# Performance work log

Hardware: AMD Instinct MI355X
Metric: run time of the kernel (lower is better)

Reference implementation:

```python
import jax, jax.numpy as jnp
import numpy as np

D_MODEL = 1024
NUM_HEADS = 16
THETA = 10000.0


def setup_inputs() -> dict:
    key = jax.random.key(0)
    ks = jax.random.split(key, 5)
    B, S, D = 4, 2048, D_MODEL
    std = float(np.sqrt(2.0 / (D + D)))
    x = jax.random.normal(ks[0], (B, S, D), dtype=jnp.float32)
    wq = jax.random.normal(ks[1], (D, D), dtype=jnp.float32) * std
    wk = jax.random.normal(ks[2], (D, D), dtype=jnp.float32) * std
    wv = jax.random.normal(ks[3], (D, D), dtype=jnp.float32) * std
    wo = jax.random.normal(ks[4], (D, D), dtype=jnp.float32) * std
    token_positions = jnp.broadcast_to(jnp.arange(S, dtype=jnp.int32), (B, S))
    return {"x": x, "token_positions": token_positions,
            "wq": wq, "wk": wk, "wv": wv, "wo": wo}


def _rope(t, token_positions, d_k):
    # t: [B, H, S, d_k]; token_positions: [B, S]
    freqs = 1.0 / (THETA ** (jnp.arange(0, d_k, 2, dtype=jnp.float32) / d_k))  # [d_k/2]
    angles = token_positions.astype(jnp.float32)[..., None] * freqs            # [B, S, d_k/2]
    angles = jnp.repeat(angles, 2, axis=-1)                                    # [B, S, d_k]
    cos = jnp.cos(angles)[:, None, :, :]  # broadcast over heads
    sin = jnp.sin(angles)[:, None, :, :]
    t1, t2 = t[..., 0::2], t[..., 1::2]
    t_rot = jnp.stack([-t2, t1], axis=-1).reshape(t.shape)  # interleave (-x2, x1)
    return t * cos + t_rot * sin


def reference(x, token_positions, wq, wk, wv, wo):
    B, S, D = x.shape
    H = NUM_HEADS
    d_k = D // H
    def proj(w):
        return (x @ w.T).reshape(B, S, H, d_k).transpose(0, 2, 1, 3)  # [B,H,S,dk]
    q = _rope(proj(wq), token_positions, d_k)
    k = _rope(proj(wk), token_positions, d_k)
    v = proj(wv)
    scale = 1.0 / jnp.sqrt(jnp.float32(d_k))
    scores = jnp.einsum('bhqd,bhkd->bhqk', q, k) * scale  # [B,H,S,S]
    causal = jnp.tril(jnp.ones((S, S), dtype=bool))
    scores = jnp.where(causal, scores, -jnp.inf)
    attn = jax.nn.softmax(scores, axis=-1)
    out = jnp.einsum('bhqk,bhkd->bhqd', attn, v)          # [B,H,S,dk]
    out = out.transpose(0, 2, 1, 3).reshape(B, S, D)
    return out @ wo.T
```

## Files before the change

### kernel.cpp

```cpp
#include <hip/hip_runtime.h>
#include <hip/hip_bf16.h>
#include <cstdint>
#include <cstddef>

#define B_ 4
#define S_ 2048
#define D_ 1024
#define H_ 16
#define DK_ 64
#define NTOK (B_*S_)

typedef __bf16 bf16;
typedef __bf16 bf16x8 __attribute__((ext_vector_type(8)));
typedef short s16x4 __attribute__((ext_vector_type(4)));
typedef float f32x4 __attribute__((ext_vector_type(4)));

#define AS1 __attribute__((address_space(1)))
#define AS3 __attribute__((address_space(3)))

static __device__ __forceinline__ short f2bf_s(float f) {
    return __builtin_bit_cast(short, (__bf16)f);
}

static __device__ __forceinline__ f32x4 mfma16(s16x4 a, s16x4 b, f32x4 c) {
#if __has_builtin(__builtin_amdgcn_mfma_f32_16x16x16bf16_1k)
    return __builtin_amdgcn_mfma_f32_16x16x16bf16_1k(a, b, c, 0, 0, 0);
#else
    asm volatile("v_mfma_f32_16x16x16_bf16 %0, %1, %2, %0\n\ts_nop 7\n\ts_nop 7"
                 : "+v"(c) : "v"(a), "v"(b));
    return c;
#endif
}

__global__ void cvt_all(const float* __restrict__ x, const float* __restrict__ wq,
                        const float* __restrict__ wk, const float* __restrict__ wv,
                        const float* __restrict__ wo, bf16* __restrict__ dst) {
    const int NX8 = NTOK * D_ / 8;
    const int W8 = D_ * D_ / 8;
    int i = blockIdx.x * blockDim.x + threadIdx.x;
    if (i >= NX8 + 4 * W8) return;
    const float* src; int j;
    if (i < NX8) { src = x; j = i; }
    else {
        int k = i - NX8;
        int w = k >> 17;
        j = k & (W8 - 1);
        src = w == 0 ? wq : (w == 1 ? wk : (w == 2 ? wv : wo));
    }
    const float4* s4 = reinterpret_cast<const float4*>(src) + (size_t)j * 2;
    float4 a = s4[0], b = s4[1];
    bf16x8 o;
    o[0] = (bf16)a.x; o[1] = (bf16)a.y; o[2] = (bf16)a.z; o[3] = (bf16)a.w;
    o[4] = (bf16)b.x; o[5] = (bf16)b.y; o[6] = (bf16)b.z; o[7] = (bf16)b.w;
    reinterpret_cast<bf16x8*>(dst)[i] = o;
}

__global__ void rope_table(const int* __restrict__ pos, float2* __restrict__ tab) {
    int i = blockIdx.x * blockDim.x + threadIdx.x;
    if (i >= NTOK * 32) return;
    int n = i >> 5, p = i & 31;
    float pf = (float)pos[n];
    float freq = powf(10000.0f, -(float)p * (1.0f / 32.0f));
    float ang = pf * freq;
    float s, c;
    sincosf(ang, &s, &c);
    tab[i] = make_float2(c, s);
}

__global__ __launch_bounds__(256, 2)
void gemm_qkv(const bf16* __restrict__ A, const bf16* __restrict__ Bw,
              bf16* __restrict__ Qr, bf16* __restrict__ Kz, bf16* __restrict__ VT,
              const float2* __restrict__ tab) {
    const float SCL2E = 0.125f * 1.44269504088896340736f;
    constexpr int NKT = 16;
    __shared__ alignas(16) bf16 lds[2][(128 + 128) * 64];
    const int tid = threadIdx.x;
    const int lane = tid & 63;
    const int wid = tid >> 6;
    const int wm = wid >> 1, wn = wid & 1;
    const int lr = lane & 15, lg = lane >> 4;
    const int m0 = blockIdx.x * 128;
    const int n0g = blockIdx.y * 128;

    f32x4 acc[4][4] = {};

    auto stageA = [&](int kt, int bufi) {
        bf16* dst = &lds[bufi][0];
#pragma unroll
        for (int j = 0; j < 4; ++j) {
            int flat = j * 256 + tid;
            int r = flat >> 3, c = flat & 7;
            const bf16* src = A + (size_t)(m0 + r) * 1024 + kt * 64 + ((c ^ (r & 7)) << 3);
            __builtin_amdgcn_global_load_lds((const AS1 uint32_t*)src,
                                             (AS3 uint32_t*)(dst + (size_t)flat * 8), 16, 0, 0);
        }
    };
    auto stageB = [&](int kt, int bufi) {
        bf16* dst = &lds[bufi][0] + 128 * 64;
#pragma unroll
        for (int j = 0; j < 4; ++j) {
            int flat = j * 256 + tid;
            int r = flat >> 3, c = flat & 7;
            const bf16* src = Bw + (size_t)(n0g + r) * 1024 + kt * 64 + ((c ^ (r & 7)) << 3);
            __builtin_amdgcn_global_load_lds((const AS1 uint32_t*)src,
                                             (AS3 uint32_t*)(dst + (size_t)flat * 8), 16, 0, 0);
        }
    };

    stageA(0, 0);
    stageB(0, 0);

    for (int kt = 0; kt < NKT; ++kt) {
        const bf16* bufA = &lds[kt & 1][0];
        const bf16* bufB = bufA + 128 * 64;

        asm volatile("" ::: "memory");
        __builtin_amdgcn_s_barrier();
        asm volatile("" ::: "memory");
        if (kt + 1 < NKT) {
            stageA(kt + 1, (kt + 1) & 1);
            asm volatile("s_waitcnt vmcnt(4)" ::: "memory");
        } else {
            asm volatile("s_waitcnt vmcnt(0)" ::: "memory");
        }
        __builtin_amdgcn_s_barrier();
        asm volatile("" ::: "memory");

        const int sx = lr & 7;
        bf16x8 af[4][2], bfr[4][2];
#pragma unroll
        for (int mf = 0; mf < 4; ++mf)
#pragma unroll
            for (int kh = 0; kh < 2; ++kh)
                af[mf][kh] = *reinterpret_cast<const bf16x8*>(
                    &bufA[(wm * 64 + mf * 16 + lr) * 64 + (((kh * 4 + lg) ^ sx) << 3)]);
#pragma unroll
        for (int nf = 0; nf < 2; ++nf)
#pragma unroll
            for (int kh = 0; kh < 2; ++kh)
                bfr[nf][kh] = *reinterpret_cast<const bf16x8*>(
                    &bufB[(wn * 64 + nf * 16 + lr) * 64 + (((kh * 4 + lg) ^ sx) << 3)]);
        __builtin_amdgcn_s_setprio(1);
#pragma unroll
        for (int mf = 0; mf < 4; ++mf)
#pragma unroll
            for (int nf = 0; nf < 2; ++nf)
#pragma unroll
                for (int kh = 0; kh < 2; ++kh)
                    acc[mf][nf] = __builtin_amdgcn_mfma_f32_16x16x32_bf16(af[mf][kh], bfr[nf][kh], acc[mf][nf], 0, 0, 0);
        __builtin_amdgcn_s_setprio(0);
        if (kt + 1 < NKT) stageB(kt + 1, (kt + 1) & 1);
        asm volatile("" ::: "memory");
        __builtin_amdgcn_s_barrier();
        asm volatile("" ::: "memory");
#pragma unroll
        for (int nf = 2; nf < 4; ++nf)
#pragma unroll
            for (int kh = 0; kh < 2; ++kh)
                bfr[nf][kh] = *reinterpret_cast<const bf16x8*>(
                    &bufB[(wn * 64 + nf * 16 + lr) * 64 + (((kh * 4 + lg) ^ sx) << 3)]);
        __builtin_amdgcn_s_setprio(1);
#pragma unroll
        for (int mf = 0; mf < 4; ++mf)
#pragma unroll
            for (int nf = 2; nf < 4; ++nf)
#pragma unroll
                for (int kh = 0; kh < 2; ++kh)
                    acc[mf][nf] = __builtin_amdgcn_mfma_f32_16x16x32_bf16(af[mf][kh], bfr[nf][kh], acc[mf][nf], 0, 0, 0);
        __builtin_amdgcn_s_setprio(0);
    }

#pragma unroll
    for (int mf = 0; mf < 4; ++mf) {
#pragma unroll
        for (int nf = 0; nf < 4; ++nf) {
            int row0 = m0 + wm * 64 + mf * 16 + lg * 4;
            int colg = n0g + wn * 64 + nf * 16 + lr;
            int which = colg >> 10;
            int col = colg & 1023;
            if (which < 2) {
#pragma unroll
                for (int r = 0; r < 4; ++r) {
                    int row = row0 + r;
                    float v = acc[mf][nf][r];
                    float partner = __shfl_xor(v, 1, 64);
                    float2 cs = tab[(size_t)row * 32 + ((col >> 1) & 31)];
                    float o = (col & 1) ? fmaf(v, cs.x, partner * cs.y)
                                        : fmaf(v, cs.x, -partner * cs.y);
                    if (which == 0) {
                        Qr[(size_t)row * 1024 + col] = (bf16)(o * SCL2E);
                    } else {
                        int h = col >> 6, e = col & 63;
                        int e2 = e ^ ((row & 7) << 3);
                        Kz[(size_t)row * 1024 + h * 64 + e2] = (bf16)o;
                    }
                }
            } else {
                int h = col >> 6, dd = col & 63;
                int kvb = row0 & 63;
                int sw = (((dd & 7) ^ ((dd >> 3) & 7)) & 7) << 3;
                s16x4 pk;
#pragma unroll
                for (int r = 0; r < 4; ++r) pk[r] = f2bf_s(acc[mf][nf][r]);
                size_t addr = ((((size_t)((row0 >> 11) * 16 + h)) * 32 + ((row0 >> 6) & 31)) * 64 + dd) * 64
                              + (size_t)(kvb ^ sw);
                *reinterpret_cast<s16x4*>(&VT[addr]) = pk;
            }
        }
    }
}

__global__ __launch_bounds__(256, 2)
void gemm_out(const bf16* __restrict__ A, const bf16* __restrict__ Bw,
              float* __restrict__ Cp) {
    constexpr int NKT = 16;
    __shared__ alignas(16) bf16 lds[2][(128 + 128) * 64];
    const int tid = threadIdx.x;
    const int lane = tid & 63;
    const int wid = tid >> 6;
    const int wm = wid >> 1, wn = wid & 1;
    const int lr = lane & 15, lg = lane >> 4;
    const int m0 = blockIdx.x * 128;
    const int n0g = blockIdx.y * 128;

    f32x4 acc[4][4] = {};

    auto stageA = [&](int kt, int bufi) {
        bf16* dst = &lds[bufi][0];
#pragma unroll
        for (int j = 0; j < 4; ++j) {
            int flat = j * 256 + tid;
            int r = flat >> 3, c = flat & 7;
            const bf16* src = A + (size_t)(m0 + r) * 1024 + kt * 64 + ((c ^ (r & 7)) << 3);
            __builtin_amdgcn_global_load_lds((const AS1 uint32_t*)src,
                                             (AS3 uint32_t*)(dst + (size_t)flat * 8), 16, 0, 0);
        }
    };
    auto stageB = [&](int kt, int bufi) {
        bf16* dst = &lds[bufi][0] + 128 * 64;
#pragma unroll
        for (int j = 0; j < 4; ++j) {
            int flat = j * 256 + tid;
            int r = flat >> 3, c = flat & 7;
            const bf16* src = Bw + (size_t)(n0g + r) * 1024 + kt * 64 + ((c ^ (r & 7)) << 3);
            __builtin_amdgcn_global_load_lds((const AS1 uint32_t*)src,
                                             (AS3 uint32_t*)(dst + (size_t)flat * 8), 16, 0, 0);
        }
    };

    stageA(0, 0);
    stageB(0, 0);

    for (int kt = 0; kt < NKT; ++kt) {
        const bf16* bufA = &lds[kt & 1][0];
        const bf16* bufB = bufA + 128 * 64;

        asm volatile("" ::: "memory");
        __builtin_amdgcn_s_barrier();
        asm volatile("" ::: "memory");
        if (kt + 1 < NKT) {
            stageA(kt + 1, (kt + 1) & 1);
            asm volatile("s_waitcnt vmcnt(4)" ::: "memory");
        } else {
            asm volatile("s_waitcnt vmcnt(0)" ::: "memory");
        }
        __builtin_amdgcn_s_barrier();
        asm volatile("" ::: "memory");

        const int sx = lr & 7;
        bf16x8 af[4][2], bfr[4][2];
#pragma unroll
        for (int mf = 0; mf < 4; ++mf)
#pragma unroll
            for (int kh = 0; kh < 2; ++kh)
                af[mf][kh] = *reinterpret_cast<const bf16x8*>(
                    &bufA[(wm * 64 + mf * 16 + lr) * 64 + (((kh * 4 + lg) ^ sx) << 3)]);
#pragma unroll
        for (int nf = 0; nf < 2; ++nf)
#pragma unroll
            for (int kh = 0; kh < 2; ++kh)
                bfr[nf][kh] = *reinterpret_cast<const bf16x8*>(
                    &bufB[(wn * 64 + nf * 16 + lr) * 64 + (((kh * 4 + lg) ^ sx) << 3)]);
        __builtin_amdgcn_s_setprio(1);
#pragma unroll
        for (int mf = 0; mf < 4; ++mf)
#pragma unroll
            for (int nf = 0; nf < 2; ++nf)
#pragma unroll
                for (int kh = 0; kh < 2; ++kh)
                    acc[mf][nf] = __builtin_amdgcn_mfma_f32_16x16x32_bf16(af[mf][kh], bfr[nf][kh], acc[mf][nf], 0, 0, 0);
        __builtin_amdgcn_s_setprio(0);
        if (kt + 1 < NKT) stageB(kt + 1, (kt + 1) & 1);
        asm volatile("" ::: "memory");
        __builtin_amdgcn_s_barrier();
        asm volatile("" ::: "memory");
#pragma unroll
        for (int nf = 2; nf < 4; ++nf)
#pragma unroll
            for (int kh = 0; kh < 2; ++kh)
                bfr[nf][kh] = *reinterpret_cast<const bf16x8*>(
                    &bufB[(wn * 64 + nf * 16 + lr) * 64 + (((kh * 4 + lg) ^ sx) << 3)]);
        __builtin_amdgcn_s_setprio(1);
#pragma unroll
        for (int mf = 0; mf < 4; ++mf)
#pragma unroll
            for (int nf = 2; nf < 4; ++nf)
#pragma unroll
                for (int kh = 0; kh < 2; ++kh)
                    acc[mf][nf] = __builtin_amdgcn_mfma_f32_16x16x32_bf16(af[mf][kh], bfr[nf][kh], acc[mf][nf], 0, 0, 0);
        __builtin_amdgcn_s_setprio(0);
    }

#pragma unroll
    for (int mf = 0; mf < 4; ++mf)
#pragma unroll
        for (int nf = 0; nf < 4; ++nf)
#pragma unroll
            for (int r = 0; r < 4; ++r) {
                int row = m0 + wm * 64 + mf * 16 + lg * 4 + r;
                int colg = n0g + wn * 64 + nf * 16 + lr;
                Cp[(size_t)row * 1024 + colg] = acc[mf][nf][r];
            }
}

__global__ __launch_bounds__(256, 2)
void flash_attn11(const bf16* __restrict__ Q, const bf16* __restrict__ Kz,
                  const bf16* __restrict__ VT, bf16* __restrict__ O) {
    __shared__ bf16 Ks[2][64 * 64];
    __shared__ bf16 Vt[2][64 * 64];
    const int tid = threadIdx.x, lane = tid & 63, w = tid >> 6;
    const int lr = lane & 15, lg = lane >> 4;
    const int qtA = blockIdx.x;
    const int qtB = 15 - qtA;
    const int q0[2] = { qtA * 128, qtB * 128 };
    const int ntS[2] = { 2 * qtA + 2, 2 * qtB + 2 };
    const int NT = ntS[1];
    const int bh = blockIdx.y;
    const int b = bh >> 4, h = bh & 15;
    const size_t base = ((size_t)b * S_) * D_ + (size_t)h * DK_;
    const size_t vtbase = (size_t)bh * 32 * 4096;

    bf16x8 aq[2][2][2];
#pragma unroll
    for (int si = 0; si < 2; ++si)
#pragma unroll
        for (int qs = 0; qs < 2; ++qs) {
            int qrow = q0[si] + w * 32 + qs * 16 + lr;
            const bf16* qp = Q + base + (size_t)qrow * D_ + lg * 8;
            aq[si][qs][0] = *reinterpret_cast<const bf16x8*>(qp);
            aq[si][qs][1] = *reinterpret_cast<const bf16x8*>(qp + 32);
        }

    f32x4 acc[2][2][4] = {};
    f32x4 l_acc[2][2] = {};
    float m_run[2][2] = {{-1e30f, -1e30f}, {-1e30f, -1e30f}};

    const short ONEB = (short)0x3F80;
    const s16x4 ones = { ONEB, ONEB, ONEB, ONEB };

    const int sjj = tid >> 3;
    const int se0 = (tid & 7) * 8;

    auto stage = [&](int t, int bufi) {
        bf16* kd = Ks[bufi];
        bf16* vd = Vt[bufi];
#pragma unroll
        for (int i = 0; i < 2; ++i) {
            int jj = sjj + i * 32;
            const bf16* ksrc = Kz + base + (size_t)(t * 64 + jj) * 1024 + se0;
            __builtin_amdgcn_global_load_lds((const AS1 uint32_t*)ksrc,
                                             (AS3 uint32_t*)(kd + jj * 64 + se0), 16, 0, 0);
            const bf16* vsrc = VT + vtbase + (size_t)t * 4096 + jj * 64 + se0;
            __builtin_amdgcn_global_load_lds((const AS1 uint32_t*)vsrc,
                                             (AS3 uint32_t*)(vd + jj * 64 + se0), 16, 0, 0);
        }
    };

    stage(0, 0);

    for (int t = 0; t < NT; ++t) {
        const int j0 = t * 64;
        const bf16* KsB = Ks[t & 1];
        const bf16* VtB = Vt[t & 1];

        asm volatile("" ::: "memory");
        __builtin_amdgcn_s_barrier();
        asm volatile("" ::: "memory");
        if (t + 1 < NT) {
            stage(t + 1, (t + 1) & 1);
            asm volatile("s_waitcnt vmcnt(4)" ::: "memory");
        } else {
            asm volatile("s_waitcnt vmcnt(0)" ::: "memory");
        }
        __builtin_amdgcn_s_barrier();
        asm volatile("" ::: "memory");

        const bool act[2] = { t < ntS[0] && j0 <= q0[0] + w * 32 + 31,
                              j0 <= q0[1] + w * 32 + 31 };
        f32x4 sc[2][2][4];

        __builtin_amdgcn_s_setprio(1);
#pragma unroll
        for (int si = 0; si < 2; ++si) {
            if (!act[si]) continue;
#pragma unroll
            for (int nt = 0; nt < 4; ++nt) {
                int krow = nt * 16 + lr;
                int swz = (krow & 7) << 3;
                bf16x8 a0 = *reinterpret_cast<const bf16x8*>(&KsB[krow * 64 + ((lg * 8) ^ swz)]);
                bf16x8 a1 = *reinterpret_cast<const bf16x8*>(&KsB[krow * 64 + ((32 + lg * 8) ^ swz)]);
#pragma unroll
                for (int qs = 0; qs < 2; ++qs) {
                    f32x4 tv = {};
                    tv = __builtin_amdgcn_mfma_f32_16x16x32_bf16(a0, aq[si][qs][0], tv, 0, 0, 0);
                    tv = __builtin_amdgcn_mfma_f32_16x16x32_bf16(a1, aq[si][qs][1], tv, 0, 0, 0);
                    sc[si][qs][nt] = tv;
                }
            }
        }
        __builtin_amdgcn_s_setprio(0);

#pragma unroll
        for (int si = 0; si < 2; ++si) {
            if (!act[si]) continue;

            s16x4 ap[2][4];
#pragma unroll
            for (int qs = 0; qs < 2; ++qs) {
                const int qrow = q0[si] + w * 32 + qs * 16 + lr;
                if (j0 + 63 > q0[si] + w * 32 + qs * 16) {
#pragma unroll
                    for (int nt = 0; nt < 4; ++nt)
#pragma unroll
                        for (int r = 0; r < 4; ++r) {
                            int kv = j0 + nt * 16 + lg * 4 + r;
                            if (kv > qrow) sc[si][qs][nt][r] = -1e30f;
                        }
                }
                float tmax = sc[si][qs][0][0];
#pragma unroll
                for (int nt = 0; nt < 4; ++nt)
#pragma unroll
                    for (int r = 0; r < 4; ++r) tmax = fmaxf(tmax, sc[si][qs][nt][r]);
                tmax = fmaxf(tmax, __shfl_xor(tmax, 16, 64));
                tmax = fmaxf(tmax, __shfl_xor(tmax, 32, 64));
                float mold = m_run[si][qs];
                if (!__all(tmax - mold <= 8.0f)) {
                    float mnew = fmaxf(mold, tmax);
                    float corr = exp2f(mold - mnew);
                    m_run[si][qs] = mnew;
#pragma unroll
                    for (int r = 0; r < 4; ++r) {
                        float cr = __shfl(corr, (lane & 48) | (lg * 4 + r), 64);
                        l_acc[si][qs][r] *= cr;
#pragma unroll
                        for (int dt = 0; dt < 4; ++dt) acc[si][qs][dt][r] *= cr;
                    }
                }
                float mnow = m_run[si][qs];
#pragma unroll
                for (int nt = 0; nt < 4; ++nt) {
                    float p0 = exp2f(sc[si][qs][nt][0] - mnow);
                    float p1 = exp2f(sc[si][qs][nt][1] - mnow);
                    float p2 = exp2f(sc[si][qs][nt][2] - mnow);
                    float p3 = exp2f(sc[si][qs][nt][3] - mnow);
                    int ulo, uhi;
                    asm("v_cvt_pk_bf16_f32 %0, %1, %2" : "=v"(ulo) : "v"(p0), "v"(p1));
                    asm("v_cvt_pk_bf16_f32 %0, %1, %2" : "=v"(uhi) : "v"(p2), "v"(p3));
                    int2 pr; pr.x = ulo; pr.y = uhi;
                    ap[qs][nt] = __builtin_bit_cast(s16x4, pr);
                }
            }

            __builtin_amdgcn_s_setprio(1);
#pragma unroll
            for (int qs = 0; qs < 2; ++qs)
#pragma unroll
                for (int nt = 0; nt < 4; ++nt)
                    l_acc[si][qs] = mfma16(ap[qs][nt], ones, l_acc[si][qs]);
#pragma unroll
            for (int dt = 0; dt < 4; ++dt) {
                int vrow = dt * 16 + lr;
                int vswz = (((vrow & 7) ^ (vrow >> 3)) & 7) << 3;
                s16x4 bv[4];
#pragma unroll
                for (int nt = 0; nt < 4; ++nt)
                    bv[nt] = *reinterpret_cast<const s16x4*>(&VtB[vrow * 64 + ((nt * 16 + lg * 4) ^ vswz)]);
#pragma unroll
                for (int qs = 0; qs < 2; ++qs)
#pragma unroll
                    for (int nt = 0; nt < 4; ++nt)
                        acc[si][qs][dt] = mfma16(ap[qs][nt], bv[nt], acc[si][qs][dt]);
            }
            __builtin_amdgcn_s_setprio(0);
        }
    }

#pragma unroll
    for (int si = 0; si < 2; ++si)
#pragma unroll
        for (int qs = 0; qs < 2; ++qs)
#pragma unroll
            for (int r = 0; r < 4; ++r) {
                float invr = __builtin_amdgcn_rcpf(l_acc[si][qs][r]);
                int row = q0[si] + w * 32 + qs * 16 + lg * 4 + r;
#pragma unroll
                for (int dt = 0; dt < 4; ++dt)
                    O[base + (size_t)row * D_ + dt * 16 + lr] = (bf16)(acc[si][qs][dt][r] * invr);
            }
}

extern "C" void kernel_launch(void* const* d_in, const int* in_sizes, int n_in,
                              void* d_out, int out_size, void* d_ws, size_t ws_size,
                              hipStream_t stream) {
    const float* x  = (const float*)d_in[0];
    const int*   tp = (const int*)d_in[1];
    const float* wq = (const float*)d_in[2];
    const float* wk = (const float*)d_in[3];
    const float* wv = (const float*)d_in[4];
    const float* wo = (const float*)d_in[5];

    bf16* ws = (bf16*)d_ws;
    bf16* Xbf = ws;
    bf16* Wqb = Xbf + (size_t)NTOK * D_;
    bf16* Wkb = Wqb + (size_t)D_ * D_;
    bf16* Wvb = Wkb + (size_t)D_ * D_;
    bf16* Wob = Wvb + (size_t)D_ * D_;
    bf16* Qr  = Wob + (size_t)D_ * D_;
    bf16* Kz  = Qr + (size_t)NTOK * D_;
    bf16* VT  = Kz + (size_t)NTOK * D_;
    bf16* AO  = VT + (size_t)NTOK * D_;
    float2* tab = (float2*)(AO + (size_t)NTOK * D_);
    (void)ws_size; (void)in_sizes; (void)n_in; (void)out_size;
    (void)Wkb; (void)Wvb;

    {
        int ntot8 = (NTOK * D_ + 4 * D_ * D_) / 8;
        cvt_all<<<(ntot8 + 255) / 256, 256, 0, stream>>>(x, wq, wk, wv, wo, Xbf);
    }
    rope_table<<<(NTOK * 32 + 255) / 256, 256, 0, stream>>>(tp, tab);

    gemm_qkv<<<dim3(NTOK / 128, 24), 256, 0, stream>>>(Xbf, Wqb, Qr, Kz, VT, tab);

    flash_attn11<<<dim3(8, B_ * H_), 256, 0, stream>>>(Qr, Kz, VT, AO);

    gemm_out<<<dim3(NTOK / 128, D_ / 128), 256, 0, stream>>>(AO, Wob, (float*)d_out);
}
```

Baseline: 206.9 us.

## Split attention work over 8 waves per block and merge cvt with rope table

The flash attention kernel now launches 512 threads per block, so each wave handles 16 query rows per tile instead of 32. This halves per-thread register state and raises the number of waves available to hide latency. Only the first 256 threads issue the K/V LDS staging loads. Separately, the bf16 conversion and RoPE table kernels are merged into one launch to save a kernel launch. The risks are lower MFMA reuse of each K/V fragment per wave and heavier barrier synchronisation across 8 waves.

```diff
diff --git a/kernel.cpp b/kernel.cpp
--- a/kernel.cpp
+++ b/kernel.cpp
@@ -32,39 +32,40 @@
 #endif
 }
 
-__global__ void cvt_all(const float* __restrict__ x, const float* __restrict__ wq,
-                        const float* __restrict__ wk, const float* __restrict__ wv,
-                        const float* __restrict__ wo, bf16* __restrict__ dst) {
+__global__ void cvt_rope(const float* __restrict__ x, const float* __restrict__ wq,
+                         const float* __restrict__ wk, const float* __restrict__ wv,
+                         const float* __restrict__ wo, const int* __restrict__ pos,
+                         bf16* __restrict__ dst, float2* __restrict__ tab) {
     const int NX8 = NTOK * D_ / 8;
     const int W8 = D_ * D_ / 8;
+    const int NCVT = NX8 + 4 * W8;
     int i = blockIdx.x * blockDim.x + threadIdx.x;
-    if (i >= NX8 + 4 * W8) return;
-    const float* src; int j;
-    if (i < NX8) { src = x; j = i; }
-    else {
-        int k = i - NX8;
-        int w = k >> 17;
-        j = k & (W8 - 1);
-        src = w == 0 ? wq : (w == 1 ? wk : (w == 2 ? wv : wo));
-    }
-    const float4* s4 = reinterpret_cast<const float4*>(src) + (size_t)j * 2;
-    float4 a = s4[0], b = s4[1];
-    bf16x8 o;
-    o[0] = (bf16)a.x; o[1] = (bf16)a.y; o[2] = (bf16)a.z; o[3] = (bf16)a.w;
-    o[4] = (bf16)b.x; o[5] = (bf16)b.y; o[6] = (bf16)b.z; o[7] = (bf16)b.w;
-    reinterpret_cast<bf16x8*>(dst)[i] = o;
-}
-
-__global__ void rope_table(const int* __restrict__ pos, float2* __restrict__ tab) {
-    int i = blockIdx.x * blockDim.x + threadIdx.x;
-    if (i >= NTOK * 32) return;
-    int n = i >> 5, p = i & 31;
-    float pf = (float)pos[n];
-    float freq = powf(10000.0f, -(float)p * (1.0f / 32.0f));
-    float ang = pf * freq;
-    float s, c;
-    sincosf(ang, &s, &c);
-    tab[i] = make_float2(c, s);
+    if (i < NCVT) {
+        const float* src; int j;
+        if (i < NX8) { src = x; j = i; }
+        else {
+            int k = i - NX8;
+            int w = k >> 17;
+            j = k & (W8 - 1);
+            src = w == 0 ? wq : (w == 1 ? wk : (w == 2 ? wv : wo));
+        }
+        const float4* s4 = reinterpret_cast<const float4*>(src) + (size_t)j * 2;
+        float4 a = s4[0], b = s4[1];
+        bf16x8 o;
+        o[0] = (bf16)a.x; o[1] = (bf16)a.y; o[2] = (bf16)a.z; o[3] = (bf16)a.w;
+        o[4] = (bf16)b.x; o[5] = (bf16)b.y; o[6] = (bf16)b.z; o[7] = (bf16)b.w;
+        reinterpret_cast<bf16x8*>(dst)[i] = o;
+    } else {
+        int k = i - NCVT;
+        if (k >= NTOK * 32) return;
+        int n = k >> 5, p = k & 31;
+        float pf = (float)pos[n];
+        float freq = powf(10000.0f, -(float)p * (1.0f / 32.0f));
+        float ang = pf * freq;
+        float s, c;
+        sincosf(ang, &s, &c);
+        tab[k] = make_float2(c, s);
+    }
 }
 
 __global__ __launch_bounds__(256, 2)
@@ -323,8 +324,8 @@
             }
 }
 
-__global__ __launch_bounds__(256, 2)
-void flash_attn11(const bf16* __restrict__ Q, const bf16* __restrict__ Kz,
+__global__ __launch_bounds__(512)
+void flash_attn13(const bf16* __restrict__ Q, const bf16* __restrict__ Kz,
                   const bf16* __restrict__ VT, bf16* __restrict__ O) {
     __shared__ bf16 Ks[2][64 * 64];
     __shared__ bf16 Vt[2][64 * 64];
@@ -340,28 +341,28 @@
     const size_t base = ((size_t)b * S_) * D_ + (size_t)h * DK_;
     const size_t vtbase = (size_t)bh * 32 * 4096;
 
-    bf16x8 aq[2][2][2];
-#pragma unroll
-    for (int si = 0; si < 2; ++si)
-#pragma unroll
-        for (int qs = 0; qs < 2; ++qs) {
-            int qrow = q0[si] + w * 32 + qs * 16 + lr;
-            const bf16* qp = Q + base + (size_t)qrow * D_ + lg * 8;
-            aq[si][qs][0] = *reinterpret_cast<const bf16x8*>(qp);
-            aq[si][qs][1] = *reinterpret_cast<const bf16x8*>(qp + 32);
-        }
-
-    f32x4 acc[2][2][4] = {};
-    f32x4 l_acc[2][2] = {};
-    float m_run[2][2] = {{-1e30f, -1e30f}, {-1e30f, -1e30f}};
+    bf16x8 aq[2][2];
+#pragma unroll
+    for (int si = 0; si < 2; ++si) {
+        int qrow = q0[si] + w * 16 + lr;
+        const bf16* qp = Q + base + (size_t)qrow * D_ + lg * 8;
+        aq[si][0] = *reinterpret_cast<const bf16x8*>(qp);
+        aq[si][1] = *reinterpret_cast<const bf16x8*>(qp + 32);
+    }
+
+    f32x4 acc[2][4] = {};
+    f32x4 l_acc[2] = {};
+    float m_run[2] = {-1e30f, -1e30f};
 
     const short ONEB = (short)0x3F80;
     const s16x4 ones = { ONEB, ONEB, ONEB, ONEB };
 
     const int sjj = tid >> 3;
     const int se0 = (tid & 7) * 8;
+    const bool stager = tid < 256;
 
     auto stage = [&](int t, int bufi) {
+        if (!stager) return;
         bf16* kd = Ks[bufi];
         bf16* vd = Vt[bufi];
 #pragma unroll
@@ -395,89 +396,76 @@
         __builtin_amdgcn_s_barrier();
         asm volatile("" ::: "memory");
 
-        const bool act[2] = { t < ntS[0] && j0 <= q0[0] + w * 32 + 31,
-                              j0 <= q0[1] + w * 32 + 31 };
-        f32x4 sc[2][2][4];
-
-        __builtin_amdgcn_s_setprio(1);
 #pragma unroll
         for (int si = 0; si < 2; ++si) {
-            if (!act[si]) continue;
+            if (t >= ntS[si]) continue;
+            const int qw0 = q0[si] + w * 16;
+            if (j0 > qw0 + 15) continue;
+
+            f32x4 sc[4];
+            __builtin_amdgcn_s_setprio(1);
 #pragma unroll
             for (int nt = 0; nt < 4; ++nt) {
                 int krow = nt * 16 + lr;
                 int swz = (krow & 7) << 3;
                 bf16x8 a0 = *reinterpret_cast<const bf16x8*>(&KsB[krow * 64 + ((lg * 8) ^ swz)]);
                 bf16x8 a1 = *reinterpret_cast<const bf16x8*>(&KsB[krow * 64 + ((32 + lg * 8) ^ swz)]);
-#pragma unroll
-                for (int qs = 0; qs < 2; ++qs) {
-                    f32x4 tv = {};
-                    tv = __builtin_amdgcn_mfma_f32_16x16x32_bf16(a0, aq[si][qs][0], tv, 0, 0, 0);
-                    tv = __builtin_amdgcn_mfma_f32_16x16x32_bf16(a1, aq[si][qs][1], tv, 0, 0, 0);
-                    sc[si][qs][nt] = tv;
+                f32x4 tv = {};
+                tv = __builtin_amdgcn_mfma_f32_16x16x32_bf16(a0, aq[si][0], tv, 0, 0, 0);
+                tv = __builtin_amdgcn_mfma_f32_16x16x32_bf16(a1, aq[si][1], tv, 0, 0, 0);
+                sc[nt] = tv;
+            }
+            __builtin_amdgcn_s_setprio(0);
+
+            const int qrow = qw0 + lr;
+            if (j0 + 63 > qw0) {
+#pragma unroll
+                for (int nt = 0; nt < 4; ++nt)
+#pragma unroll
+                    for (int r = 0; r < 4; ++r) {
+                        int kv = j0 + nt * 16 + lg * 4 + r;
+                        if (kv > qrow) sc[nt][r] = -1e30f;
+                    }
+            }
+            float tmax = sc[0][0];
+#pragma unroll
+            for (int nt = 0; nt < 4; ++nt)
+#pragma unroll
+                for (int r = 0; r < 4; ++r) tmax = fmaxf(tmax, sc[nt][r]);
+            tmax = fmaxf(tmax, __shfl_xor(tmax, 16, 64));
+            tmax = fmaxf(tmax, __shfl_xor(tmax, 32, 64));
+            float mold = m_run[si];
+            if (!__all(tmax - mold <= 8.0f)) {
+                float mnew = fmaxf(mold, tmax);
+                float corr = exp2f(mold - mnew);
+                m_run[si] = mnew;
+#pragma unroll
+                for (int r = 0; r < 4; ++r) {
+                    float cr = __shfl(corr, (lane & 48) | (lg * 4 + r), 64);
+                    l_acc[si][r] *= cr;
+#pragma unroll
+                    for (int dt = 0; dt < 4; ++dt) acc[si][dt][r] *= cr;
                 }
             }
-        }
-        __builtin_amdgcn_s_setprio(0);
-
-#pragma unroll
-        for (int si = 0; si < 2; ++si) {
-            if (!act[si]) continue;
-
-            s16x4 ap[2][4];
-#pragma unroll
-            for (int qs = 0; qs < 2; ++qs) {
-                const int qrow = q0[si] + w * 32 + qs * 16 + lr;
-                if (j0 + 63 > q0[si] + w * 32 + qs * 16) {
-#pragma unroll
-                    for (int nt = 0; nt < 4; ++nt)
-#pragma unroll
-                        for (int r = 0; r < 4; ++r) {
-                            int kv = j0 + nt * 16 + lg * 4 + r;
-                            if (kv > qrow) sc[si][qs][nt][r] = -1e30f;
-                        }
-                }
-                float tmax = sc[si][qs][0][0];
-#pragma unroll
-                for (int nt = 0; nt < 4; ++nt)
-#pragma unroll
-                    for (int r = 0; r < 4; ++r) tmax = fmaxf(tmax, sc[si][qs][nt][r]);
-                tmax = fmaxf(tmax, __shfl_xor(tmax, 16, 64));
-                tmax = fmaxf(tmax, __shfl_xor(tmax, 32, 64));
-                float mold = m_run[si][qs];
-                if (!__all(tmax - mold <= 8.0f)) {
-                    float mnew = fmaxf(mold, tmax);
-                    float corr = exp2f(mold - mnew);
-                    m_run[si][qs] = mnew;
-#pragma unroll
-                    for (int r = 0; r < 4; ++r) {
-                        float cr = __shfl(corr, (lane & 48) | (lg * 4 + r), 64);
-                        l_acc[si][qs][r] *= cr;
-#pragma unroll
-                        for (int dt = 0; dt < 4; ++dt) acc[si][qs][dt][r] *= cr;
-                    }
-                }
-                float mnow = m_run[si][qs];
-#pragma unroll
-                for (int nt = 0; nt < 4; ++nt) {
-                    float p0 = exp2f(sc[si][qs][nt][0] - mnow);
-                    float p1 = exp2f(sc[si][qs][nt][1] - mnow);
-                    float p2 = exp2f(sc[si][qs][nt][2] - mnow);
-                    float p3 = exp2f(sc[si][qs][nt][3] - mnow);
-                    int ulo, uhi;
-                    asm("v_cvt_pk_bf16_f32 %0, %1, %2" : "=v"(ulo) : "v"(p0), "v"(p1));
-                    asm("v_cvt_pk_bf16_f32 %0, %1, %2" : "=v"(uhi) : "v"(p2), "v"(p3));
-                    int2 pr; pr.x = ulo; pr.y = uhi;
-                    ap[qs][nt] = __builtin_bit_cast(s16x4, pr);
-                }
+            float mnow = m_run[si];
+            s16x4 ap[4];
+#pragma unroll
+            for (int nt = 0; nt < 4; ++nt) {
+                float p0 = exp2f(sc[nt][0] - mnow);
+                float p1 = exp2f(sc[nt][1] - mnow);
+                float p2 = exp2f(sc[nt][2] - mnow);
+                float p3 = exp2f(sc[nt][3] - mnow);
+                int ulo, uhi;
+                asm("v_cvt_pk_bf16_f32 %0, %1, %2" : "=v"(ulo) : "v"(p0), "v"(p1));
+                asm("v_cvt_pk_bf16_f32 %0, %1, %2" : "=v"(uhi) : "v"(p2), "v"(p3));
+                int2 pr; pr.x = ulo; pr.y = uhi;
+                ap[nt] = __builtin_bit_cast(s16x4, pr);
             }
 
             __builtin_amdgcn_s_setprio(1);
 #pragma unroll
-            for (int qs = 0; qs < 2; ++qs)
-#pragma unroll
-                for (int nt = 0; nt < 4; ++nt)
-                    l_acc[si][qs] = mfma16(ap[qs][nt], ones, l_acc[si][qs]);
+            for (int nt = 0; nt < 4; ++nt)
+                l_acc[si] = mfma16(ap[nt], ones, l_acc[si]);
 #pragma unroll
             for (int dt = 0; dt < 4; ++dt) {
                 int vrow = dt * 16 + lr;
@@ -487,10 +475,8 @@
                 for (int nt = 0; nt < 4; ++nt)
                     bv[nt] = *reinterpret_cast<const s16x4*>(&VtB[vrow * 64 + ((nt * 16 + lg * 4) ^ vswz)]);
 #pragma unroll
-                for (int qs = 0; qs < 2; ++qs)
-#pragma unroll
-                    for (int nt = 0; nt < 4; ++nt)
-                        acc[si][qs][dt] = mfma16(ap[qs][nt], bv[nt], acc[si][qs][dt]);
+                for (int nt = 0; nt < 4; ++nt)
+                    acc[si][dt] = mfma16(ap[nt], bv[nt], acc[si][dt]);
             }
             __builtin_amdgcn_s_setprio(0);
         }
@@ -499,15 +485,13 @@
 #pragma unroll
     for (int si = 0; si < 2; ++si)
 #pragma unroll
-        for (int qs = 0; qs < 2; ++qs)
-#pragma unroll
-            for (int r = 0; r < 4; ++r) {
-                float invr = __builtin_amdgcn_rcpf(l_acc[si][qs][r]);
-                int row = q0[si] + w * 32 + qs * 16 + lg * 4 + r;
-#pragma unroll
-                for (int dt = 0; dt < 4; ++dt)
-                    O[base + (size_t)row * D_ + dt * 16 + lr] = (bf16)(acc[si][qs][dt][r] * invr);
-            }
+        for (int r = 0; r < 4; ++r) {
+            float invr = __builtin_amdgcn_rcpf(l_acc[si][r]);
+            int row = q0[si] + w * 16 + lg * 4 + r;
+#pragma unroll
+            for (int dt = 0; dt < 4; ++dt)
+                O[base + (size_t)row * D_ + dt * 16 + lr] = (bf16)(acc[si][dt][r] * invr);
+        }
 }
 
 extern "C" void kernel_launch(void* const* d_in, const int* in_sizes, int n_in,
@@ -535,14 +519,13 @@
     (void)Wkb; (void)Wvb;
 
     {
-        int ntot8 = (NTOK * D_ + 4 * D_ * D_) / 8;
-        cvt_all<<<(ntot8 + 255) / 256, 256, 0, stream>>>(x, wq, wk, wv, wo, Xbf);
-    }
-    rope_table<<<(NTOK * 32 + 255) / 256, 256, 0, stream>>>(tp, tab);
+        int ntot = (NTOK * D_ + 4 * D_ * D_) / 8 + NTOK * 32;
+        cvt_rope<<<(ntot + 255) / 256, 256, 0, stream>>>(x, wq, wk, wv, wo, tp, Xbf, tab);
+    }
 
     gemm_qkv<<<dim3(NTOK / 128, 24), 256, 0, stream>>>(Xbf, Wqb, Qr, Kz, VT, tab);
 
-    flash_attn11<<<dim3(8, B_ * H_), 256, 0, stream>>>(Qr, Kz, VT, AO);
+    flash_attn13<<<dim3(8, B_ * H_), 512, 0, stream>>>(Qr, Kz, VT, AO);
 
     gemm_out<<<dim3(NTOK / 128, D_ / 128), 256, 0, stream>>>(AO, Wob, (float*)d_out);
 }
```

New measurement: 219.6 us. 6.2% more time.

## Stage 128-key KV tiles per barrier in attention and fuse rope table into convert

Applied to the files above, without the earlier changes.

The flash attention kernel now stages two 64-key K/V tiles (128 keys) into LDS per double-buffer step. This halves the number of barrier/wait rounds and issues larger load batches, at the cost of doubling LDS use to 64KB per block, which may limit occupancy. Separately, the rope sin/cos table computation is merged into the bf16 conversion kernel to drop one launch.

```diff
diff --git a/kernel.cpp b/kernel.cpp
--- a/kernel.cpp
+++ b/kernel.cpp
@@ -32,39 +32,40 @@
 #endif
 }
 
-__global__ void cvt_all(const float* __restrict__ x, const float* __restrict__ wq,
-                        const float* __restrict__ wk, const float* __restrict__ wv,
-                        const float* __restrict__ wo, bf16* __restrict__ dst) {
+__global__ void cvt_rope(const float* __restrict__ x, const float* __restrict__ wq,
+                         const float* __restrict__ wk, const float* __restrict__ wv,
+                         const float* __restrict__ wo, const int* __restrict__ pos,
+                         bf16* __restrict__ dst, float2* __restrict__ tab) {
     const int NX8 = NTOK * D_ / 8;
     const int W8 = D_ * D_ / 8;
+    const int NCVT = NX8 + 4 * W8;
     int i = blockIdx.x * blockDim.x + threadIdx.x;
-    if (i >= NX8 + 4 * W8) return;
-    const float* src; int j;
-    if (i < NX8) { src = x; j = i; }
-    else {
-        int k = i - NX8;
-        int w = k >> 17;
-        j = k & (W8 - 1);
-        src = w == 0 ? wq : (w == 1 ? wk : (w == 2 ? wv : wo));
+    if (i < NCVT) {
+        const float* src; int j;
+        if (i < NX8) { src = x; j = i; }
+        else {
+            int k = i - NX8;
+            int w = k >> 17;
+            j = k & (W8 - 1);
+            src = w == 0 ? wq : (w == 1 ? wk : (w == 2 ? wv : wo));
+        }
+        const float4* s4 = reinterpret_cast<const float4*>(src) + (size_t)j * 2;
+        float4 a = s4[0], b = s4[1];
+        bf16x8 o;
+        o[0] = (bf16)a.x; o[1] = (bf16)a.y; o[2] = (bf16)a.z; o[3] = (bf16)a.w;
+        o[4] = (bf16)b.x; o[5] = (bf16)b.y; o[6] = (bf16)b.z; o[7] = (bf16)b.w;
+        reinterpret_cast<bf16x8*>(dst)[i] = o;
+    } else {
+        int k = i - NCVT;
+        if (k >= NTOK * 32) return;
+        int n = k >> 5, p = k & 31;
+        float pf = (float)pos[n];
+        float freq = powf(10000.0f, -(float)p * (1.0f / 32.0f));
+        float ang = pf * freq;
+        float s, c;
+        sincosf(ang, &s, &c);
+        tab[k] = make_float2(c, s);
     }
-    const float4* s4 = reinterpret_cast<const float4*>(src) + (size_t)j * 2;
-    float4 a = s4[0], b = s4[1];
-    bf16x8 o;
-    o[0] = (bf16)a.x; o[1] = (bf16)a.y; o[2] = (bf16)a.z; o[3] = (bf16)a.w;
-    o[4] = (bf16)b.x; o[5] = (bf16)b.y; o[6] = (bf16)b.z; o[7] = (bf16)b.w;
-    reinterpret_cast<bf16x8*>(dst)[i] = o;
-}
-
-__global__ void rope_table(const int* __restrict__ pos, float2* __restrict__ tab) {
-    int i = blockIdx.x * blockDim.x + threadIdx.x;
-    if (i >= NTOK * 32) return;
-    int n = i >> 5, p = i & 31;
-    float pf = (float)pos[n];
-    float freq = powf(10000.0f, -(float)p * (1.0f / 32.0f));
-    float ang = pf * freq;
-    float s, c;
-    sincosf(ang, &s, &c);
-    tab[i] = make_float2(c, s);
 }
 
 __global__ __launch_bounds__(256, 2)
@@ -324,10 +325,10 @@
 }
 
 __global__ __launch_bounds__(256, 2)
-void flash_attn11(const bf16* __restrict__ Q, const bf16* __restrict__ Kz,
+void flash_attn15(const bf16* __restrict__ Q, const bf16* __restrict__ Kz,
                   const bf16* __restrict__ VT, bf16* __restrict__ O) {
-    __shared__ bf16 Ks[2][64 * 64];
-    __shared__ bf16 Vt[2][64 * 64];
+    __shared__ bf16 Ks[2][128 * 64];
+    __shared__ bf16 Vt[2][2 * 4096];
     const int tid = threadIdx.x, lane = tid & 63, w = tid >> 6;
     const int lr = lane & 15, lg = lane >> 4;
     const int qtA = blockIdx.x;
@@ -335,6 +336,7 @@
     const int q0[2] = { qtA * 128, qtB * 128 };
     const int ntS[2] = { 2 * qtA + 2, 2 * qtB + 2 };
     const int NT = ntS[1];
+    const int NT2 = NT >> 1;
     const int bh = blockIdx.y;
     const int b = bh >> 4, h = bh & 15;
     const size_t base = ((size_t)b * S_) * D_ + (size_t)h * DK_;
@@ -361,138 +363,143 @@
     const int sjj = tid >> 3;
     const int se0 = (tid & 7) * 8;
 
-    auto stage = [&](int t, int bufi) {
+    auto stage = [&](int t2, int bufi) {
         bf16* kd = Ks[bufi];
         bf16* vd = Vt[bufi];
 #pragma unroll
-        for (int i = 0; i < 2; ++i) {
+        for (int i = 0; i < 4; ++i) {
             int jj = sjj + i * 32;
-            const bf16* ksrc = Kz + base + (size_t)(t * 64 + jj) * 1024 + se0;
+            const bf16* ksrc = Kz + base + (size_t)(t2 * 128 + jj) * 1024 + se0;
             __builtin_amdgcn_global_load_lds((const AS1 uint32_t*)ksrc,
                                              (AS3 uint32_t*)(kd + jj * 64 + se0), 16, 0, 0);
-            const bf16* vsrc = VT + vtbase + (size_t)t * 4096 + jj * 64 + se0;
-            __builtin_amdgcn_global_load_lds((const AS1 uint32_t*)vsrc,
-                                             (AS3 uint32_t*)(vd + jj * 64 + se0), 16, 0, 0);
-        }
+        }
+#pragma unroll
+        for (int s2 = 0; s2 < 2; ++s2)
+#pragma unroll
+            for (int i = 0; i < 2; ++i) {
+                int jj = sjj + i * 32;
+                const bf16* vsrc = VT + vtbase + (size_t)(t2 * 2 + s2) * 4096 + jj * 64 + se0;
+                __builtin_amdgcn_global_load_lds((const AS1 uint32_t*)vsrc,
+                                                 (AS3 uint32_t*)(vd + s2 * 4096 + jj * 64 + se0), 16, 0, 0);
+            }
     };
 
     stage(0, 0);
 
-    for (int t = 0; t < NT; ++t) {
-        const int j0 = t * 64;
-        const bf16* KsB = Ks[t & 1];
-        const bf16* VtB = Vt[t & 1];
-
-        asm volatile("" ::: "memory");
-        __builtin_amdgcn_s_barrier();
-        asm volatile("" ::: "memory");
-        if (t + 1 < NT) {
-            stage(t + 1, (t + 1) & 1);
-            asm volatile("s_waitcnt vmcnt(4)" ::: "memory");
+    for (int t2 = 0; t2 < NT2; ++t2) {
+        asm volatile("" ::: "memory");
+        __builtin_amdgcn_s_barrier();
+        asm volatile("" ::: "memory");
+        if (t2 + 1 < NT2) {
+            stage(t2 + 1, (t2 + 1) & 1);
+            asm volatile("s_waitcnt vmcnt(8)" ::: "memory");
         } else {
             asm volatile("s_waitcnt vmcnt(0)" ::: "memory");
         }
         __builtin_amdgcn_s_barrier();
         asm volatile("" ::: "memory");
 
-        const bool act[2] = { t < ntS[0] && j0 <= q0[0] + w * 32 + 31,
-                              j0 <= q0[1] + w * 32 + 31 };
-        f32x4 sc[2][2][4];
-
-        __builtin_amdgcn_s_setprio(1);
-#pragma unroll
-        for (int si = 0; si < 2; ++si) {
-            if (!act[si]) continue;
-#pragma unroll
-            for (int nt = 0; nt < 4; ++nt) {
-                int krow = nt * 16 + lr;
-                int swz = (krow & 7) << 3;
-                bf16x8 a0 = *reinterpret_cast<const bf16x8*>(&KsB[krow * 64 + ((lg * 8) ^ swz)]);
-                bf16x8 a1 = *reinterpret_cast<const bf16x8*>(&KsB[krow * 64 + ((32 + lg * 8) ^ swz)]);
-#pragma unroll
-                for (int qs = 0; qs < 2; ++qs) {
-                    f32x4 tv = {};
-                    tv = __builtin_amdgcn_mfma_f32_16x16x32_bf16(a0, aq[si][qs][0], tv, 0, 0, 0);
-                    tv = __builtin_amdgcn_mfma_f32_16x16x32_bf16(a1, aq[si][qs][1], tv, 0, 0, 0);
-                    sc[si][qs][nt] = tv;
-                }
-            }
-        }
-        __builtin_amdgcn_s_setprio(0);
-
-#pragma unroll
-        for (int si = 0; si < 2; ++si) {
-            if (!act[si]) continue;
-
-            s16x4 ap[2][4];
-#pragma unroll
-            for (int qs = 0; qs < 2; ++qs) {
-                const int qrow = q0[si] + w * 32 + qs * 16 + lr;
-                if (j0 + 63 > q0[si] + w * 32 + qs * 16) {
-#pragma unroll
-                    for (int nt = 0; nt < 4; ++nt)
-#pragma unroll
-                        for (int r = 0; r < 4; ++r) {
-                            int kv = j0 + nt * 16 + lg * 4 + r;
-                            if (kv > qrow) sc[si][qs][nt][r] = -1e30f;
-                        }
-                }
-                float tmax = sc[si][qs][0][0];
-#pragma unroll
-                for (int nt = 0; nt < 4; ++nt)
-#pragma unroll
-                    for (int r = 0; r < 4; ++r) tmax = fmaxf(tmax, sc[si][qs][nt][r]);
-                tmax = fmaxf(tmax, __shfl_xor(tmax, 16, 64));
-                tmax = fmaxf(tmax, __shfl_xor(tmax, 32, 64));
-                float mold = m_run[si][qs];
-                if (!__all(tmax - mold <= 8.0f)) {
-                    float mnew = fmaxf(mold, tmax);
-                    float corr = exp2f(mold - mnew);
-                    m_run[si][qs] = mnew;
-#pragma unroll
-                    for (int r = 0; r < 4; ++r) {
-                        float cr = __shfl(corr, (lane & 48) | (lg * 4 + r), 64);
-                        l_acc[si][qs][r] *= cr;
-#pragma unroll
-                        for (int dt = 0; dt < 4; ++dt) acc[si][qs][dt][r] *= cr;
+#pragma unroll
+        for (int s2 = 0; s2 < 2; ++s2) {
+            const int t = t2 * 2 + s2;
+            const int j0 = t * 64;
+            const bf16* KsB = Ks[t2 & 1] + s2 * 64 * 64;
+            const bf16* VtB = Vt[t2 & 1] + s2 * 4096;
+
+#pragma unroll
+            for (int si = 0; si < 2; ++si) {
+                if (t >= ntS[si]) continue;
+                const int qmaxw = q0[si] + w * 32 + 31;
+                if (j0 > qmaxw) continue;
+
+                f32x4 sc[2][4];
+                __builtin_amdgcn_s_setprio(1);
+#pragma unroll
+                for (int nt = 0; nt < 4; ++nt) {
+                    int krow = nt * 16 + lr;
+                    int swz = (krow & 7) << 3;
+                    bf16x8 a0 = *reinterpret_cast<const bf16x8*>(&KsB[krow * 64 + ((lg * 8) ^ swz)]);
+                    bf16x8 a1 = *reinterpret_cast<const bf16x8*>(&KsB[krow * 64 + ((32 + lg * 8) ^ swz)]);
+#pragma unroll
+                    for (int qs = 0; qs < 2; ++qs) {
+                        f32x4 tv = {};
+                        tv = __builtin_amdgcn_mfma_f32_16x16x32_bf16(a0, aq[si][qs][0], tv, 0, 0, 0);
+                        tv = __builtin_amdgcn_mfma_f32_16x16x32_bf16(a1, aq[si][qs][1], tv, 0, 0, 0);
+                        sc[qs][nt] = tv;
                     }
                 }
-                float mnow = m_run[si][qs];
-#pragma unroll
-                for (int nt = 0; nt < 4; ++nt) {
-                    float p0 = exp2f(sc[si][qs][nt][0] - mnow);
-                    float p1 = exp2f(sc[si][qs][nt][1] - mnow);
-                    float p2 = exp2f(sc[si][qs][nt][2] - mnow);
-                    float p3 = exp2f(sc[si][qs][nt][3] - mnow);
-                    int ulo, uhi;
-                    asm("v_cvt_pk_bf16_f32 %0, %1, %2" : "=v"(ulo) : "v"(p0), "v"(p1));
-                    asm("v_cvt_pk_bf16_f32 %0, %1, %2" : "=v"(uhi) : "v"(p2), "v"(p3));
-                    int2 pr; pr.x = ulo; pr.y = uhi;
-                    ap[qs][nt] = __builtin_bit_cast(s16x4, pr);
+                __builtin_amdgcn_s_setprio(0);
+
+                s16x4 ap[2][4];
+#pragma unroll
+                for (int qs = 0; qs < 2; ++qs) {
+                    const int qrow = q0[si] + w * 32 + qs * 16 + lr;
+                    if (j0 + 63 > q0[si] + w * 32 + qs * 16) {
+#pragma unroll
+                        for (int nt = 0; nt < 4; ++nt)
+#pragma unroll
+                            for (int r = 0; r < 4; ++r) {
+                                int kv = j0 + nt * 16 + lg * 4 + r;
+                                if (kv > qrow) sc[qs][nt][r] = -1e30f;
+                            }
+                    }
+                    float tmax = sc[qs][0][0];
+#pragma unroll
+                    for (int nt = 0; nt < 4; ++nt)
+#pragma unroll
+                        for (int r = 0; r < 4; ++r) tmax = fmaxf(tmax, sc[qs][nt][r]);
+                    tmax = fmaxf(tmax, __shfl_xor(tmax, 16, 64));
+                    tmax = fmaxf(tmax, __shfl_xor(tmax, 32, 64));
+                    float mold = m_run[si][qs];
+                    if (!__all(tmax - mold <= 8.0f)) {
+                        float mnew = fmaxf(mold, tmax);
+                        float corr = exp2f(mold - mnew);
+                        m_run[si][qs] = mnew;
+#pragma unroll
+                        for (int r = 0; r < 4; ++r) {
+                            float cr = __shfl(corr, (lane & 48) | (lg * 4 + r), 64);
+                            l_acc[si][qs][r] *= cr;
+#pragma unroll
+                            for (int dt = 0; dt < 4; ++dt) acc[si][qs][dt][r] *= cr;
+                        }
+                    }
+                    float mnow = m_run[si][qs];
+#pragma unroll
+                    for (int nt = 0; nt < 4; ++nt) {
+                        float p0 = exp2f(sc[qs][nt][0] - mnow);
+                        float p1 = exp2f(sc[qs][nt][1] - mnow);
+                        float p2 = exp2f(sc[qs][nt][2] - mnow);
+                        float p3 = exp2f(sc[qs][nt][3] - mnow);
+                        int ulo, uhi;
+                        asm("v_cvt_pk_bf16_f32 %0, %1, %2" : "=v"(ulo) : "v"(p0), "v"(p1));
+                        asm("v_cvt_pk_bf16_f32 %0, %1, %2" : "=v"(uhi) : "v"(p2), "v"(p3));
+                        int2 pr; pr.x = ulo; pr.y = uhi;
+                        ap[qs][nt] = __builtin_bit_cast(s16x4, pr);
+                    }
                 }
+
+                __builtin_amdgcn_s_setprio(1);
+#pragma unroll
+                for (int qs = 0; qs < 2; ++qs)
+#pragma unroll
+                    for (int nt = 0; nt < 4; ++nt)
+                        l_acc[si][qs] = mfma16(ap[qs][nt], ones, l_acc[si][qs]);
+#pragma unroll
+                for (int dt = 0; dt < 4; ++dt) {
+                    int vrow = dt * 16 + lr;
+                    int vswz = (((vrow & 7) ^ (vrow >> 3)) & 7) << 3;
+                    s16x4 bv[4];
+#pragma unroll
+                    for (int nt = 0; nt < 4; ++nt)
+                        bv[nt] = *reinterpret_cast<const s16x4*>(&VtB[vrow * 64 + ((nt * 16 + lg * 4) ^ vswz)]);
+#pragma unroll
+                    for (int qs = 0; qs < 2; ++qs)
+#pragma unroll
+                        for (int nt = 0; nt < 4; ++nt)
+                            acc[si][qs][dt] = mfma16(ap[qs][nt], bv[nt], acc[si][qs][dt]);
+                }
+                __builtin_amdgcn_s_setprio(0);
             }
-
-            __builtin_amdgcn_s_setprio(1);
-#pragma unroll
-            for (int qs = 0; qs < 2; ++qs)
-#pragma unroll
-                for (int nt = 0; nt < 4; ++nt)
-                    l_acc[si][qs] = mfma16(ap[qs][nt], ones, l_acc[si][qs]);
-#pragma unroll
-            for (int dt = 0; dt < 4; ++dt) {
-                int vrow = dt * 16 + lr;
-                int vswz = (((vrow & 7) ^ (vrow >> 3)) & 7) << 3;
-                s16x4 bv[4];
-#pragma unroll
-                for (int nt = 0; nt < 4; ++nt)
-                    bv[nt] = *reinterpret_cast<const s16x4*>(&VtB[vrow * 64 + ((nt * 16 + lg * 4) ^ vswz)]);
-#pragma unroll
-                for (int qs = 0; qs < 2; ++qs)
-#pragma unroll
-                    for (int nt = 0; nt < 4; ++nt)
-                        acc[si][qs][dt] = mfma16(ap[qs][nt], bv[nt], acc[si][qs][dt]);
-            }
-            __builtin_amdgcn_s_setprio(0);
         }
     }
 
@@ -535,14 +542,13 @@
     (void)Wkb; (void)Wvb;
 
     {
-        int ntot8 = (NTOK * D_ + 4 * D_ * D_) / 8;
-        cvt_all<<<(ntot8 + 255) / 256, 256, 0, stream>>>(x, wq, wk, wv, wo, Xbf);
+        int ntot = (NTOK * D_ + 4 * D_ * D_) / 8 + NTOK * 32;
+        cvt_rope<<<(ntot + 255) / 256, 256, 0, stream>>>(x, wq, wk, wv, wo, tp, Xbf, tab);
     }
-    rope_table<<<(NTOK * 32 + 255) / 256, 256, 0, stream>>>(tp, tab);
 
     gemm_qkv<<<dim3(NTOK / 128, 24), 256, 0, stream>>>(Xbf, Wqb, Qr, Kz, VT, tab);
 
-    flash_attn11<<<dim3(8, B_ * H_), 256, 0, stream>>>(Qr, Kz, VT, AO);
+    flash_attn15<<<dim3(8, B_ * H_), 256, 0, stream>>>(Qr, Kz, VT, AO);
 
     gemm_out<<<dim3(NTOK / 128, D_ / 128), 256, 0, stream>>>(AO, Wob, (float*)d_out);
 }
```

Result: no change. 204.6 us (-1.1%).
